# Kernel optimization log

Measured on AMD Instinct MI355X. Metric: run time of the kernel, lower is better.

Reference implementation:

```python
import math
import jax, jax.numpy as jnp
import numpy as np

B, T, C, H = 4, 2048, 1024, 16
HS = C // H


def setup_inputs() -> dict:
    key = jax.random.key(0)
    ks = jax.random.split(key, 5)
    s_in = 1.0 / math.sqrt(C)
    return {
        "x": jax.random.normal(ks[0], (B, T, C), dtype=jnp.float32),
        "w_attn": jax.random.normal(ks[1], (C, 3 * C), dtype=jnp.float32) * s_in,
        "b_attn": jax.random.normal(ks[2], (3 * C,), dtype=jnp.float32) * 0.02,
        "w_proj": jax.random.normal(ks[3], (C, C), dtype=jnp.float32) * s_in,
        "b_proj": jax.random.normal(ks[4], (C,), dtype=jnp.float32) * 0.02,
    }


def reference(x, w_attn, b_attn, w_proj, b_proj):
    Bx, Tx, Cx = x.shape
    hs = Cx // H
    qkv = x @ w_attn + b_attn  # [B, T, 3C]
    q, k, v = jnp.split(qkv, 3, axis=-1)
    # [B, H, T, hs]
    q = q.reshape(Bx, Tx, H, hs).transpose(0, 2, 1, 3)
    k = k.reshape(Bx, Tx, H, hs).transpose(0, 2, 1, 3)
    v = v.reshape(Bx, Tx, H, hs).transpose(0, 2, 1, 3)
    scale = 1.0 / math.sqrt(hs)
    att = jnp.einsum("bhqd,bhkd->bhqk", q, k) * scale  # [B, H, T, T]
    causal = jnp.tril(jnp.ones((Tx, Tx), dtype=bool))
    att = jnp.where(causal, att, -jnp.inf)
    att = jax.nn.softmax(att, axis=-1)
    y = jnp.einsum("bhqk,bhkd->bhqd", att, v)  # [B, H, T, hs]
    y = y.transpose(0, 2, 1, 3).reshape(Bx, Tx, Cx)
    return y @ w_proj + b_proj
```

## Files before the change

kernel.cpp:

```cpp
#include <hip/hip_runtime.h>
#include <stdint.h>

#define Bn 4
#define Tn 2048
#define Cn 1024
#define Hn 16
#define HSn 64
#define Mn (Bn*Tn)
#define N1n (3*Cn)

typedef unsigned short u16;
typedef unsigned int u32;
typedef __attribute__((ext_vector_type(8))) short short8;
typedef __attribute__((ext_vector_type(4))) float f32x4;
typedef __attribute__((ext_vector_type(16))) float f32x16;

__device__ __forceinline__ u16 f2bf(float f){
  u32 u = __float_as_uint(f);
  u += 0x7fffu + ((u >> 16) & 1u);
  return (u16)(u >> 16);
}

__device__ __forceinline__ u32 pkbf(float lo, float hi_){
  u32 r; asm("v_cvt_pk_bf16_f32 %0, %1, %2" : "=v"(r) : "v"(lo), "v"(hi_)); return r;
}

__device__ __forceinline__ float fexp2(float x){
  float r; asm("v_exp_f32 %0, %1" : "=v"(r) : "v"(x)); return r;
}

__device__ __forceinline__ void plswap(u32 &a, u32 &b){
  auto r = __builtin_amdgcn_permlane32_swap(a, b, false, false);
  a = r[0]; b = r[1];
}

__device__ __forceinline__ void gload_lds16(const void* g, void* l){
  __builtin_amdgcn_global_load_lds(
      (const __attribute__((address_space(1))) u32*)g,
      (__attribute__((address_space(3))) u32*)l, 16, 0, 0);
}

#define BARRIER() __builtin_amdgcn_s_barrier()
#define WAITLGKM() asm volatile("s_waitcnt lgkmcnt(0)" ::: "memory")

__global__ void k_cvt(const float* __restrict__ in, u16* __restrict__ out, int n8){
  int i = blockIdx.x*256 + threadIdx.x;
  if (i >= n8) return;
  const float4* p = (const float4*)(in) + (size_t)i*2;
  float4 a = p[0], b = p[1];
  uint4 r;
  r.x = (u32)f2bf(a.x) | ((u32)f2bf(a.y) << 16);
  r.y = (u32)f2bf(a.z) | ((u32)f2bf(a.w) << 16);
  r.z = (u32)f2bf(b.x) | ((u32)f2bf(b.y) << 16);
  r.w = (u32)f2bf(b.z) | ((u32)f2bf(b.w) << 16);
  *((uint4*)(out) + i) = r;
}

__global__ void k_tcvt(const float* __restrict__ in, u16* __restrict__ out, int R, int Cc){
  __shared__ float sh[64][68];
  int tid = threadIdx.x;
  int c0 = blockIdx.x*64, r0 = blockIdx.y*64;
  int rr = tid >> 4, c4 = (tid & 15) * 4;
  #pragma unroll
  for (int p=0;p<4;p++){
    int r = rr + 16*p;
    *(float4*)&sh[r][c4] = *(const float4*)&in[(size_t)(r0+r)*Cc + c0 + c4];
  }
  __syncthreads();
  #pragma unroll
  for (int p=0;p<4;p++){
    int oc = rr + 16*p;
    u32 w0 = (u32)f2bf(sh[c4+0][oc]) | ((u32)f2bf(sh[c4+1][oc]) << 16);
    u32 w1 = (u32)f2bf(sh[c4+2][oc]) | ((u32)f2bf(sh[c4+3][oc]) << 16);
    uint2 pk; pk.x = w0; pk.y = w1;
    *(uint2*)&out[(size_t)(c0+oc)*R + r0 + c4] = pk;
  }
}

template <int OUT_BF16>
__global__ __launch_bounds__(512, 1)
void k_gemm8(const u16* __restrict__ A, const u16* __restrict__ Bt,
             const float* __restrict__ bias, void* __restrict__ Cout,
             int Nn_, int nx)
{
  extern __shared__ char smem[];
  const int nkt = 16;
  int tid = threadIdx.x;
  int wave = tid >> 6, lane = tid & 63, g = lane >> 4, cl = lane & 15;
  int wm = wave >> 1, wn = wave & 1;

  int nwg = gridDim.x;
  int cpx = nwg >> 3;
  int wg = (blockIdx.x & 7) * cpx + (blockIdx.x >> 3);
  int bx = wg % nx, by = wg / nx;
  int m0 = by * 256, n0 = bx * 128;

  int srow = tid >> 3;
  int scolb = (tid & 7) << 4;
  int ssw = scolb ^ ((srow & 7) << 4);
  const char* Agp = (const char*)A  + (size_t)(m0 + srow) * 2048 + ssw;
  const char* Bgp = (const char*)Bt + (size_t)(n0 + srow) * 2048 + ssw;
  char* AsL = smem;
  char* BsL = smem + 65536;

  #define SA(t_,u_) gload_lds16(Agp + (size_t)(u_)*131072 + (size_t)(t_)*128, \
                                AsL + (((t_)&1)<<15) + ((u_)<<13) + (wave<<10))
  #define SB(t_,u_) gload_lds16(Bgp + (size_t)(u_)*131072 + (size_t)(t_)*128, \
                                BsL + (((t_)&1)<<14) + ((u_)<<13) + (wave<<10))

  f32x4 acc[4][4];
  #pragma unroll
  for (int i=0;i<4;i++)
    #pragma unroll
    for (int j=0;j<4;j++) acc[i][j] = (f32x4){0.f,0.f,0.f,0.f};

  SA(0,0); SA(0,1); SA(0,2);
  SA(0,3); SB(0,0); SB(0,1);
  SA(1,0); SA(1,1); SA(1,2);
  asm volatile("s_waitcnt vmcnt(3)" ::: "memory");
  BARRIER();

  for (int t=0; t<nkt; ++t){
    const char* Asb = smem + ((t&1)<<15);
    const char* Bsb = smem + 65536 + ((t&1)<<14);
    short8 a[4][2], bq[2][2];
    #pragma unroll
    for (int i=0;i<4;i++){
      int row = wm*64 + i*16 + cl;
      #pragma unroll
      for (int ks=0;ks<2;ks++)
        a[i][ks] = *(const short8*)(Asb + row*128 + ((ks*64 + g*16) ^ ((row&7)<<4)));
    }
    #pragma unroll
    for (int j=0;j<2;j++){
      int row = wn*64 + j*16 + cl;
      #pragma unroll
      for (int ks=0;ks<2;ks++)
        bq[j][ks] = *(const short8*)(Bsb + row*128 + ((ks*64 + g*16) ^ ((row&7)<<4)));
    }
    if (t+1 < nkt){ SA(t+1,3); SB(t+1,0); SB(t+1,1); }
    BARRIER(); WAITLGKM();
    __builtin_amdgcn_s_setprio(1);
    #pragma unroll
    for (int ks=0;ks<2;ks++)
      #pragma unroll
      for (int i=0;i<4;i++)
        #pragma unroll
        for (int j=0;j<2;j++)
          acc[i][j] = __builtin_amdgcn_mfma_f32_16x16x32_bf16(a[i][ks], bq[j][ks], acc[i][j], 0, 0, 0);
    __builtin_amdgcn_s_setprio(0);
    BARRIER();
    #pragma unroll
    for (int j=0;j<2;j++){
      int row = wn*64 + 32 + j*16 + cl;
      #pragma unroll
      for (int ks=0;ks<2;ks++)
        bq[j][ks] = *(const short8*)(Bsb + row*128 + ((ks*64 + g*16) ^ ((row&7)<<4)));
    }
    if (t+2 < nkt){
      SA(t+2,0); SA(t+2,1); SA(t+2,2);
      asm volatile("s_waitcnt vmcnt(3)" ::: "memory");
    } else {
      asm volatile("s_waitcnt vmcnt(0)" ::: "memory");
    }
    BARRIER(); WAITLGKM();
    __builtin_amdgcn_s_setprio(1);
    #pragma unroll
    for (int ks=0;ks<2;ks++)
      #pragma unroll
      for (int i=0;i<4;i++)
        #pragma unroll
        for (int j=0;j<2;j++)
          acc[i][2+j] = __builtin_amdgcn_mfma_f32_16x16x32_bf16(a[i][ks], bq[j][ks], acc[i][2+j], 0, 0, 0);
    __builtin_amdgcn_s_setprio(0);
    BARRIER();
  }
  #undef SA
  #undef SB

  #pragma unroll
  for (int jj=0;jj<4;jj++){
    int col = n0 + wn*64 + jj*16 + cl;
    float bj = bias[col];
    #pragma unroll
    for (int i=0;i<4;i++){
      int rowb = m0 + wm*64 + i*16 + g*4;
      #pragma unroll
      for (int r=0;r<4;r++){
        float v = acc[i][jj][r] + bj;
        if (OUT_BF16) ((u16*)Cout)[(size_t)(rowb+r)*Nn_ + col] = f2bf(v);
        else          ((float*)Cout)[(size_t)(rowb+r)*Nn_ + col] = v;
      }
    }
  }
}

__global__ void k_tv(const u16* __restrict__ qkv, u16* __restrict__ vt){
  __shared__ __align__(16) u16 sh[64][80];
  int tid = threadIdx.x;
  int tt = blockIdx.x * 64, bh = blockIdx.y;
  int b = bh >> 4, h = bh & 15;
  const u16* src = qkv + (size_t)(b*Tn + tt)*N1n + 2*Cn + h*HSn;
  int r = tid >> 3, c8 = (tid & 7) * 8;
  #pragma unroll
  for (int p=0;p<2;p++){
    int rr2 = r + 32*p;
    *(uint4*)&sh[rr2][c8] = *(const uint4*)&src[(size_t)rr2*N1n + c8];
  }
  __syncthreads();
  u16* dst = vt + (size_t)bh*HSn*Tn + tt;
  #pragma unroll
  for (int p=0;p<2;p++){
    int d = r + 32*p;
    u32 w0 = (u32)sh[c8+0][d] | ((u32)sh[c8+1][d] << 16);
    u32 w1 = (u32)sh[c8+2][d] | ((u32)sh[c8+3][d] << 16);
    u32 w2 = (u32)sh[c8+4][d] | ((u32)sh[c8+5][d] << 16);
    u32 w3 = (u32)sh[c8+6][d] | ((u32)sh[c8+7][d] << 16);
    uint4 pk; pk.x=w0; pk.y=w1; pk.z=w2; pk.w=w3;
    *(uint4*)&dst[(size_t)d*Tn + c8] = pk;
  }
}

__global__ __launch_bounds__(256, 4)
void k_attn(const u16* __restrict__ qkv, const u16* __restrict__ vt, u16* __restrict__ yb){
  __shared__ __align__(16) u16 Ks[2][64*64];
  __shared__ __align__(16) u16 Vs[2][64*64];
  int tid = threadIdx.x, wave = tid >> 6, lane = tid & 63;
  int ql = lane & 31, hi = lane >> 5;
  int blk = blockIdx.x;
  int xcd = blk & 7, rest = blk >> 3;
  int bh  = xcd + 8*(rest & 7);
  int qt  = 15 - (rest >> 3);
  int b = bh >> 4, h = bh & 15;

  const u16* Kbase = qkv + (size_t)b*Tn*N1n + Cn + h*HSn;
  const u16* Vbase = vt  + (size_t)bh*HSn*Tn;

  auto STAGE = [&](int bufi, int kt){
    int kb_ = kt*64;
    #pragma unroll
    for (int it=0; it<2; ++it){
      int off = it*4096 + tid*16;
      int row = off >> 7;
      int cb  = off & 127;
      int gc  = (cb ^ ((row & 7) << 4)) >> 1;
      gload_lds16(Kbase + (size_t)(kb_ + row)*N1n + gc,
                  (char*)&Ks[bufi][0] + it*4096 + (wave << 10));
      gload_lds16(Vbase + (size_t)row*Tn + kb_ + gc,
                  (char*)&Vs[bufi][0] + it*4096 + (wave << 10));
    }
  };

  const float QSC = 0.125f * 1.44269504f;

  int q0 = qt * 128;
  int qw0 = q0 + wave*32;
  int qg  = qw0 + ql;
  int ntiles = 2*qt + 2;

  const u16* Qp = qkv + (size_t)(b*Tn + qg)*N1n + h*HSn;
  short8 qf[4];
  #pragma unroll
  for (int dc=0; dc<4; ++dc){
    union { short8 v; u32 w[4]; } qa;
    qa.v = *(const short8*)&Qp[dc*16 + hi*8];
    #pragma unroll
    for (int t=0; t<4; ++t){
      u32 w = qa.w[t];
      float lo = __uint_as_float(w << 16);
      float hf = __uint_as_float(w & 0xffff0000u);
      qa.w[t] = pkbf(lo*QSC, hf*QSC);
    }
    qf[dc] = qa.v;
  }

  f32x16 accO[2];
  #pragma unroll
  for (int f=0; f<2; ++f)
    #pragma unroll
    for (int r=0; r<16; ++r) accO[f][r] = 0.f;
  float m_ = -1e30f, l_ = 0.f;

  STAGE(0, 0);
  asm volatile("s_waitcnt vmcnt(0)" ::: "memory");
  __syncthreads();
  int buf = 0;

  for (int kt=0; kt<ntiles; ++kt){
    if (kt+1 < ntiles) STAGE(buf^1, kt+1);
    const char* Ksb = (const char*)&Ks[buf][0];
    const char* Vsb = (const char*)&Vs[buf][0];
    #pragma unroll
    for (int ksub=0; ksub<2; ++ksub){
      int kbase = kt*64 + ksub*32;
      if (kbase <= qw0 + 31){
        f32x16 s;
        #pragma unroll
        for (int r=0; r<16; ++r) s[r] = 0.f;
        __builtin_amdgcn_s_setprio(1);
        #pragma unroll
        for (int dc=0; dc<4; ++dc){
          short8 kf = *(const short8*)(Ksb + ((ksub*32 + ql) << 7)
                          + ((dc*32 + hi*16) ^ ((ql & 7) << 4)));
          s = __builtin_amdgcn_mfma_f32_32x32x16_bf16(kf, qf[dc], s, 0, 0, 0);
        }
        __builtin_amdgcn_s_setprio(0);
        float p[16];
        if (kbase + 31 > qw0){
          #pragma unroll
          for (int r=0; r<16; ++r){
            int krow = kbase + (r&3) + 8*(r>>2) + 4*hi;
            p[r] = (krow > qg) ? -1e30f : s[r];
          }
        } else {
          #pragma unroll
          for (int r=0; r<16; ++r) p[r] = s[r];
        }
        float t0 = fmaxf(fmaxf(fmaxf(p[0],p[1]),fmaxf(p[2],p[3])),
                         fmaxf(fmaxf(p[4],p[5]),fmaxf(p[6],p[7])));
        float t1 = fmaxf(fmaxf(fmaxf(p[8],p[9]),fmaxf(p[10],p[11])),
                         fmaxf(fmaxf(p[12],p[13]),fmaxf(p[14],p[15])));
        float tm = fmaxf(t0, t1);
        { u32 ua = __float_as_uint(tm), ub = ua; plswap(ua, ub);
          tm = fmaxf(__uint_as_float(ua), __uint_as_float(ub)); }
        if (!__all(tm - m_ <= 8.0f)){
          float mn = fmaxf(m_, tm);
          float al = fexp2(m_ - mn);
          m_ = mn; l_ *= al;
          #pragma unroll
          for (int f=0; f<2; ++f)
            #pragma unroll
            for (int r=0; r<16; ++r) accO[f][r] *= al;
        }
        float ls = 0.f;
        #pragma unroll
        for (int r=0; r<16; ++r){ float e = fexp2(p[r] - m_); p[r] = e; ls += e; }
        { u32 ua = __float_as_uint(ls), ub = ua; plswap(ua, ub);
          l_ += __uint_as_float(ua) + __uint_as_float(ub); }
        #pragma unroll
        for (int ks=0; ks<2; ++ks){
          int pb = ks*8;
          u32 w0 = pkbf(p[pb+0], p[pb+1]);
          u32 w1 = pkbf(p[pb+2], p[pb+3]);
          u32 w2 = pkbf(p[pb+4], p[pb+5]);
          u32 w3 = pkbf(p[pb+6], p[pb+7]);
          plswap(w0, w2);
          plswap(w1, w3);
          union { u32 w[4]; short8 v; } pu;
          pu.w[0] = w0; pu.w[1] = w1; pu.w[2] = w2; pu.w[3] = w3;
          __builtin_amdgcn_s_setprio(1);
          #pragma unroll
          for (int f=0; f<2; ++f){
            short8 vf = *(const short8*)(Vsb + ((f*32 + ql) << 7)
                            + ((ksub*64 + ks*32 + hi*16) ^ ((ql & 7) << 4)));
            accO[f] = __builtin_amdgcn_mfma_f32_32x32x16_bf16(vf, pu.v, accO[f], 0, 0, 0);
          }
          __builtin_amdgcn_s_setprio(0);
        }
      }
    }
    asm volatile("s_waitcnt vmcnt(0)" ::: "memory");
    __syncthreads();
    buf ^= 1;
  }

  float rl = 1.0f / l_;
  u16* yp = yb + (size_t)(b*Tn + qg)*Cn + h*HSn;
  #pragma unroll
  for (int f=0; f<2; ++f)
    #pragma unroll
    for (int rq=0; rq<4; ++rq){
      int d0 = f*32 + rq*8 + hi*4;
      float v0 = accO[f][rq*4+0]*rl, v1 = accO[f][rq*4+1]*rl;
      float v2 = accO[f][rq*4+2]*rl, v3 = accO[f][rq*4+3]*rl;
      uint2 pk2;
      pk2.x = (u32)f2bf(v0) | ((u32)f2bf(v1) << 16);
      pk2.y = (u32)f2bf(v2) | ((u32)f2bf(v3) << 16);
      *(uint2*)&yp[d0] = pk2;
    }
}

extern "C" void kernel_launch(void* const* d_in, const int* in_sizes, int n_in,
                              void* d_out, int out_size, void* d_ws, size_t ws_size,
                              hipStream_t stream)
{
  const float* x      = (const float*)d_in[0];
  const float* w_attn = (const float*)d_in[1];
  const float* b_attn = (const float*)d_in[2];
  const float* w_proj = (const float*)d_in[3];
  const float* b_proj = (const float*)d_in[4];
  float* out = (float*)d_out;
  char* ws = (char*)d_ws;

  size_t off = 0;
  u16* xb  = (u16*)(ws + off); off += (size_t)Mn*Cn*2;
  u16* waT = (u16*)(ws + off); off += (size_t)N1n*Cn*2;
  u16* wpT = (u16*)(ws + off); off += (size_t)Cn*Cn*2;
  u16* qkv = (u16*)(ws + off); off += (size_t)Mn*N1n*2;
  u16* vt  = (u16*)(ws + off); off += (size_t)Bn*Hn*HSn*Tn*2;
  u16* yb  = (u16*)(ws + off); off += (size_t)Mn*Cn*2;

  (void)hipFuncSetAttribute((const void*)k_gemm8<1>,
        hipFuncAttributeMaxDynamicSharedMemorySize, 98304);
  (void)hipFuncSetAttribute((const void*)k_gemm8<0>,
        hipFuncAttributeMaxDynamicSharedMemorySize, 98304);

  k_cvt<<<dim3(Mn*Cn/8/256), 256, 0, stream>>>(x, xb, Mn*Cn/8);
  k_tcvt<<<dim3(N1n/64, Cn/64), 256, 0, stream>>>(w_attn, waT, Cn, N1n);
  k_tcvt<<<dim3(Cn/64, Cn/64), 256, 0, stream>>>(w_proj, wpT, Cn, Cn);
  k_gemm8<1><<<dim3((Mn/256)*(N1n/128)), 512, 98304, stream>>>(xb, waT, b_attn, qkv, N1n, N1n/128);
  k_tv<<<dim3(Tn/64, Bn*Hn), 256, 0, stream>>>(qkv, vt);
  k_attn<<<dim3(1024), 256, 0, stream>>>(qkv, vt, yb);
  k_gemm8<0><<<dim3((Mn/256)*(Cn/128)), 512, 98304, stream>>>(yb, wpT, b_proj, out, Cn, Cn/128);
}
```

Baseline: 163.6 us.

## Triple-buffer GEMM with one barrier per k-step and fuse V transpose into epilogue

```diff
diff --git a/kernel.cpp b/kernel.cpp
--- a/kernel.cpp
+++ b/kernel.cpp
@@ -41,7 +41,7 @@
 }
 
 #define BARRIER() __builtin_amdgcn_s_barrier()
-#define WAITLGKM() asm volatile("s_waitcnt lgkmcnt(0)" ::: "memory")
+#define CFENCE() asm volatile("" ::: "memory")
 
 __global__ void k_cvt(const float* __restrict__ in, u16* __restrict__ out, int n8){
   int i = blockIdx.x*256 + threadIdx.x;
@@ -77,11 +77,11 @@
   }
 }
 
-template <int OUT_BF16>
+template <int MODE>
 __global__ __launch_bounds__(512, 1)
-void k_gemm8(const u16* __restrict__ A, const u16* __restrict__ Bt,
-             const float* __restrict__ bias, void* __restrict__ Cout,
-             int Nn_, int nx)
+void k_gemm1p(const u16* __restrict__ A, const u16* __restrict__ Bt,
+              const float* __restrict__ bias, void* __restrict__ Cout,
+              u16* __restrict__ vt, int Nn_)
 {
   extern __shared__ char smem[];
   const int nkt = 16;
@@ -89,10 +89,9 @@
   int wave = tid >> 6, lane = tid & 63, g = lane >> 4, cl = lane & 15;
   int wm = wave >> 1, wn = wave & 1;
 
-  int nwg = gridDim.x;
-  int cpx = nwg >> 3;
-  int wg = (blockIdx.x & 7) * cpx + (blockIdx.x >> 3);
-  int bx = wg % nx, by = wg / nx;
+  int blk = blockIdx.x;
+  int by = ((blk & 7) << 2) + ((blk >> 3) & 3);
+  int bx = ((blk >> 5) & 7) + ((blk >> 8) << 3);
   int m0 = by * 256, n0 = bx * 128;
 
   int srow = tid >> 3;
@@ -100,13 +99,18 @@
   int ssw = scolb ^ ((srow & 7) << 4);
   const char* Agp = (const char*)A  + (size_t)(m0 + srow) * 2048 + ssw;
   const char* Bgp = (const char*)Bt + (size_t)(n0 + srow) * 2048 + ssw;
-  char* AsL = smem;
-  char* BsL = smem + 65536;
-
-  #define SA(t_,u_) gload_lds16(Agp + (size_t)(u_)*131072 + (size_t)(t_)*128, \
-                                AsL + (((t_)&1)<<15) + ((u_)<<13) + (wave<<10))
-  #define SB(t_,u_) gload_lds16(Bgp + (size_t)(u_)*131072 + (size_t)(t_)*128, \
-                                BsL + (((t_)&1)<<14) + ((u_)<<13) + (wave<<10))
+
+  #define STAGE6(t_) { int bb_ = (t_)%3; \
+    char* ab_ = smem + bb_*32768 + (wave<<10); \
+    const char* ag_ = Agp + (size_t)(t_)*128; \
+    gload_lds16(ag_,          ab_); \
+    gload_lds16(ag_+131072,   ab_+8192); \
+    gload_lds16(ag_+262144,   ab_+16384); \
+    gload_lds16(ag_+393216,   ab_+24576); \
+    char* bbp_ = smem + 98304 + bb_*16384 + (wave<<10); \
+    const char* bg_ = Bgp + (size_t)(t_)*128; \
+    gload_lds16(bg_,          bbp_); \
+    gload_lds16(bg_+131072,   bbp_+8192); }
 
   f32x4 acc[4][4];
   #pragma unroll
@@ -114,16 +118,21 @@
     #pragma unroll
     for (int j=0;j<4;j++) acc[i][j] = (f32x4){0.f,0.f,0.f,0.f};
 
-  SA(0,0); SA(0,1); SA(0,2);
-  SA(0,3); SB(0,0); SB(0,1);
-  SA(1,0); SA(1,1); SA(1,2);
-  asm volatile("s_waitcnt vmcnt(3)" ::: "memory");
-  BARRIER();
+  STAGE6(0);
+  STAGE6(1);
+  asm volatile("s_waitcnt vmcnt(6)" ::: "memory");
+  BARRIER(); CFENCE();
 
   for (int t=0; t<nkt; ++t){
-    const char* Asb = smem + ((t&1)<<15);
-    const char* Bsb = smem + 65536 + ((t&1)<<14);
-    short8 a[4][2], bq[2][2];
+    if (t+2 < nkt){
+      STAGE6(t+2);
+      asm volatile("s_waitcnt vmcnt(6)" ::: "memory");
+    } else {
+      asm volatile("s_waitcnt vmcnt(0)" ::: "memory");
+    }
+    const char* Asb = smem + (t%3)*32768;
+    const char* Bsb = smem + 98304 + (t%3)*16384;
+    short8 a[4][2], bq[4][2];
     #pragma unroll
     for (int i=0;i<4;i++){
       int row = wm*64 + i*16 + cl;
@@ -132,92 +141,58 @@
         a[i][ks] = *(const short8*)(Asb + row*128 + ((ks*64 + g*16) ^ ((row&7)<<4)));
     }
     #pragma unroll
-    for (int j=0;j<2;j++){
+    for (int j=0;j<4;j++){
       int row = wn*64 + j*16 + cl;
       #pragma unroll
       for (int ks=0;ks<2;ks++)
         bq[j][ks] = *(const short8*)(Bsb + row*128 + ((ks*64 + g*16) ^ ((row&7)<<4)));
     }
-    if (t+1 < nkt){ SA(t+1,3); SB(t+1,0); SB(t+1,1); }
-    BARRIER(); WAITLGKM();
     __builtin_amdgcn_s_setprio(1);
     #pragma unroll
     for (int ks=0;ks<2;ks++)
       #pragma unroll
       for (int i=0;i<4;i++)
         #pragma unroll
-        for (int j=0;j<2;j++)
+        for (int j=0;j<4;j++)
           acc[i][j] = __builtin_amdgcn_mfma_f32_16x16x32_bf16(a[i][ks], bq[j][ks], acc[i][j], 0, 0, 0);
     __builtin_amdgcn_s_setprio(0);
-    BARRIER();
-    #pragma unroll
-    for (int j=0;j<2;j++){
-      int row = wn*64 + 32 + j*16 + cl;
-      #pragma unroll
-      for (int ks=0;ks<2;ks++)
-        bq[j][ks] = *(const short8*)(Bsb + row*128 + ((ks*64 + g*16) ^ ((row&7)<<4)));
-    }
-    if (t+2 < nkt){
-      SA(t+2,0); SA(t+2,1); SA(t+2,2);
-      asm volatile("s_waitcnt vmcnt(3)" ::: "memory");
-    } else {
-      asm volatile("s_waitcnt vmcnt(0)" ::: "memory");
-    }
-    BARRIER(); WAITLGKM();
-    __builtin_amdgcn_s_setprio(1);
-    #pragma unroll
-    for (int ks=0;ks<2;ks++)
-      #pragma unroll
-      for (int i=0;i<4;i++)
-        #pragma unroll
-        for (int j=0;j<2;j++)
-          acc[i][2+j] = __builtin_amdgcn_mfma_f32_16x16x32_bf16(a[i][ks], bq[j][ks], acc[i][2+j], 0, 0, 0);
-    __builtin_amdgcn_s_setprio(0);
-    BARRIER();
-  }
-  #undef SA
-  #undef SB
+    CFENCE(); BARRIER(); CFENCE();
+  }
+  #undef STAGE6
 
   #pragma unroll
   for (int jj=0;jj<4;jj++){
     int col = n0 + wn*64 + jj*16 + cl;
     float bj = bias[col];
-    #pragma unroll
-    for (int i=0;i<4;i++){
-      int rowb = m0 + wm*64 + i*16 + g*4;
-      #pragma unroll
-      for (int r=0;r<4;r++){
-        float v = acc[i][jj][r] + bj;
-        if (OUT_BF16) ((u16*)Cout)[(size_t)(rowb+r)*Nn_ + col] = f2bf(v);
-        else          ((float*)Cout)[(size_t)(rowb+r)*Nn_ + col] = v;
+    if (MODE == 0){
+      #pragma unroll
+      for (int i=0;i<4;i++){
+        int rowb = m0 + wm*64 + i*16 + g*4;
+        #pragma unroll
+        for (int r=0;r<4;r++)
+          ((float*)Cout)[(size_t)(rowb+r)*Nn_ + col] = acc[i][jj][r] + bj;
       }
-    }
-  }
-}
-
-__global__ void k_tv(const u16* __restrict__ qkv, u16* __restrict__ vt){
-  __shared__ __align__(16) u16 sh[64][80];
-  int tid = threadIdx.x;
-  int tt = blockIdx.x * 64, bh = blockIdx.y;
-  int b = bh >> 4, h = bh & 15;
-  const u16* src = qkv + (size_t)(b*Tn + tt)*N1n + 2*Cn + h*HSn;
-  int r = tid >> 3, c8 = (tid & 7) * 8;
-  #pragma unroll
-  for (int p=0;p<2;p++){
-    int rr2 = r + 32*p;
-    *(uint4*)&sh[rr2][c8] = *(const uint4*)&src[(size_t)rr2*N1n + c8];
-  }
-  __syncthreads();
-  u16* dst = vt + (size_t)bh*HSn*Tn + tt;
-  #pragma unroll
-  for (int p=0;p<2;p++){
-    int d = r + 32*p;
-    u32 w0 = (u32)sh[c8+0][d] | ((u32)sh[c8+1][d] << 16);
-    u32 w1 = (u32)sh[c8+2][d] | ((u32)sh[c8+3][d] << 16);
-    u32 w2 = (u32)sh[c8+4][d] | ((u32)sh[c8+5][d] << 16);
-    u32 w3 = (u32)sh[c8+6][d] | ((u32)sh[c8+7][d] << 16);
-    uint4 pk; pk.x=w0; pk.y=w1; pk.z=w2; pk.w=w3;
-    *(uint4*)&dst[(size_t)d*Tn + c8] = pk;
+    } else if (col < 2*Cn){
+      #pragma unroll
+      for (int i=0;i<4;i++){
+        int rowb = m0 + wm*64 + i*16 + g*4;
+        #pragma unroll
+        for (int r=0;r<4;r++)
+          ((u16*)Cout)[(size_t)(rowb+r)*Nn_ + col] = f2bf(acc[i][jj][r] + bj);
+      }
+    } else {
+      int hd = col - 2*Cn;
+      #pragma unroll
+      for (int i=0;i<4;i++){
+        int rowb = m0 + wm*64 + i*16 + g*4;
+        int bb = rowb >> 11, tt = rowb & 2047;
+        u16* dst = vt + (((size_t)(bb*16 + (hd>>6)))*64 + (hd&63))*2048 + tt;
+        uint2 pk;
+        pk.x = (u32)f2bf(acc[i][jj][0]+bj) | ((u32)f2bf(acc[i][jj][1]+bj) << 16);
+        pk.y = (u32)f2bf(acc[i][jj][2]+bj) | ((u32)f2bf(acc[i][jj][3]+bj) << 16);
+        *(uint2*)dst = pk;
+      }
+    }
   }
 }
 
@@ -400,16 +375,15 @@
   u16* vt  = (u16*)(ws + off); off += (size_t)Bn*Hn*HSn*Tn*2;
   u16* yb  = (u16*)(ws + off); off += (size_t)Mn*Cn*2;
 
-  (void)hipFuncSetAttribute((const void*)k_gemm8<1>,
-        hipFuncAttributeMaxDynamicSharedMemorySize, 98304);
-  (void)hipFuncSetAttribute((const void*)k_gemm8<0>,
-        hipFuncAttributeMaxDynamicSharedMemorySize, 98304);
+  (void)hipFuncSetAttribute((const void*)k_gemm1p<1>,
+        hipFuncAttributeMaxDynamicSharedMemorySize, 147456);
+  (void)hipFuncSetAttribute((const void*)k_gemm1p<0>,
+        hipFuncAttributeMaxDynamicSharedMemorySize, 147456);
 
   k_cvt<<<dim3(Mn*Cn/8/256), 256, 0, stream>>>(x, xb, Mn*Cn/8);
   k_tcvt<<<dim3(N1n/64, Cn/64), 256, 0, stream>>>(w_attn, waT, Cn, N1n);
   k_tcvt<<<dim3(Cn/64, Cn/64), 256, 0, stream>>>(w_proj, wpT, Cn, Cn);
-  k_gemm8<1><<<dim3((Mn/256)*(N1n/128)), 512, 98304, stream>>>(xb, waT, b_attn, qkv, N1n, N1n/128);
-  k_tv<<<dim3(Tn/64, Bn*Hn), 256, 0, stream>>>(qkv, vt);
+  k_gemm1p<1><<<dim3((Mn/256)*(N1n/128)), 512, 147456, stream>>>(xb, waT, b_attn, qkv, vt, N1n);
   k_attn<<<dim3(1024), 256, 0, stream>>>(qkv, vt, yb);
-  k_gemm8<0><<<dim3((Mn/256)*(Cn/128)), 512, 98304, stream>>>(yb, wpT, b_proj, out, Cn, Cn/128);
-}
+  k_gemm1p<0><<<dim3((Mn/256)*(Cn/128)), 512, 147456, stream>>>(yb, wpT, b_proj, out, nullptr, Cn);
+}
```

Result: faster. 156.7 us (-4.2%).
